# Kernel tuning notes

Hardware: AMD Instinct MI355X
Metric: run time of the kernel (lower is better)

## Reference

```python
import jax, jax.numpy as jnp
import numpy as np

B, N, T, F_IN, H, OUT = 64, 207, 48, 6, 64, 1
RANK = 24  # fixed inner dim of learned adjacency factors


def setup_inputs() -> dict:
    key = jax.random.key(0)
    ks = jax.random.split(key, 10)
    s = lambda k, shp, sc=1.0: jax.random.normal(k, shp, jnp.float32) * sc
    return {
        "x": s(ks[0], (B, N, T, F_IN)),
        "N1": s(ks[1], (N, RANK)),
        "N2": s(ks[2], (RANK, N)),
        "W1": s(ks[3], (F_IN, H), 0.2),
        "b1": jnp.zeros((H,), jnp.float32),
        "W2": s(ks[4], (H, H), 0.1),
        "b2": jnp.zeros((H,), jnp.float32),
        "W_ih": s(ks[5], (4 * H, H), 0.1),
        "W_hh": s(ks[6], (4 * H, H), 0.1),
        "b_ih": jnp.zeros((4 * H,), jnp.float32),
        "b_hh": jnp.zeros((4 * H,), jnp.float32),
        "W_fc": s(ks[7], (H, OUT), 0.1),
        "b_fc": jnp.zeros((OUT,), jnp.float32),
    }


def reference(x, N1, N2, W1, b1, W2, b2, W_ih, W_hh, b_ih, b_hh, W_fc, b_fc):
    Bn, Nn, Tn, Fn = x.shape
    # sigmoid(N1@N2) > 0 everywhere -> dense_to_sparse yields ALL N^2 edges
    # (self-loops included); GCNConv's gcn_norm adds one extra self-loop,
    # edge weights all 1 -> A = ones + I, deg = N+1, symmetric normalization.
    adj = jax.nn.sigmoid(N1 @ N2)
    mask = (adj > 0).astype(x.dtype)  # structurally all-ones
    A = mask + jnp.eye(Nn, dtype=x.dtype)
    dinv = jax.lax.rsqrt(A.sum(axis=1))
    A_hat = dinv[:, None] * A * dinv[None, :]  # [N, N]

    xt = jnp.transpose(x, (0, 2, 1, 3))  # [B, T, N, F]
    # GCNConv: propagate(x @ W) with sym-norm, then bias; relu; dropout=eval no-op
    h = jax.nn.relu(jnp.einsum('mn,btnh->btmh', A_hat, xt @ W1) + b1)
    h = jax.nn.relu(jnp.einsum('mn,btnh->btmh', A_hat, h @ W2) + b2)

    # [B, T, N, H] -> [B*N, T, H] for the LSTM
    seq = jnp.transpose(h, (0, 2, 1, 3)).reshape(Bn * Nn, Tn, -1)
    Hd = W_hh.shape[1]

    def step(carry, x_t):
        h_prev, c_prev = carry
        g = x_t @ W_ih.T + b_ih + h_prev @ W_hh.T + b_hh
        i, f, gg, o = jnp.split(g, 4, axis=-1)  # torch gate order i,f,g,o
        c = jax.nn.sigmoid(f) * c_prev + jax.nn.sigmoid(i) * jnp.tanh(gg)
        h_new = jax.nn.sigmoid(o) * jnp.tanh(c)
        return (h_new, c), None

    h0 = jnp.zeros((Bn * Nn, Hd), x.dtype)
    (hT, _), _ = jax.lax.scan(step, (h0, h0), jnp.transpose(seq, (1, 0, 2)))
    out = hT @ W_fc + b_fc  # [B*N, OUT]
    return out.reshape(Bn, Nn, -1)
```

## Files before the change

kernel.cpp:

```cpp
#include <hip/hip_runtime.h>
#include <math.h>

#define NB 64
#define NN 207
#define NT 48
#define NF 6
#define NH 64
#define NSEQ (NB*NN)
#define NG2  (NSEQ/32)
#define TSU  ((size_t)NSEQ*NH)

typedef short bf8_t __attribute__((ext_vector_type(8)));
typedef float f4_t  __attribute__((ext_vector_type(4)));
typedef unsigned short ushort;
typedef unsigned int uint;

__device__ __forceinline__ ushort bf16h(float x){
  uint u = __float_as_uint(x);
  return (ushort)((u + 0x7FFF + ((u>>16)&1)) >> 16);
}
__device__ __forceinline__ float bf16f(ushort h){
  return __uint_as_float((uint)h << 16);
}
__device__ __forceinline__ float fsig(float x){
  return __builtin_amdgcn_rcpf(1.0f + __expf(-x));
}
__device__ __forceinline__ float ftanh(float x){
  x = fminf(15.0f, fmaxf(-15.0f, x));
  float e = __expf(2.0f*x);
  return 1.0f - 2.0f*__builtin_amdgcn_rcpf(e + 1.0f);
}

__device__ __forceinline__ void lds_barrier(){
  __builtin_amdgcn_sched_barrier(0);
  asm volatile("s_waitcnt lgkmcnt(0)" ::: "memory");
  __builtin_amdgcn_s_barrier();
  __builtin_amdgcn_sched_barrier(0);
}


#define HW 72
#define XS6 40
#define GCN7_LDS_BYTES (208*HW*2 + (207*XS6 + NF*64 + 64 + 64 + 6*64 + 6*64 + 48)*4)

__global__ __launch_bounds__(256, 2) void gcn_kernel(
    const float* __restrict__ x, const float* __restrict__ W1, const float* __restrict__ b1,
    const float* __restrict__ W2, const float* __restrict__ b2,
    ushort* __restrict__ sxh, ushort* __restrict__ sxl)
{
  extern __shared__ char smraw[];
  ushort* h1b = (ushort*)smraw;
  float*  xs6 = (float*)(h1b + 208*HW);
  float*  W1s = xs6 + 207*XS6;
  float*  b1s = W1s + NF*64;
  float*  b2s = b1s + 64;
  float*  S2_ = b2s + 64;
  float*  r1_ = S2_ + 6*64;
  float*  xsA = r1_ + 6*64;

  const int tid = threadIdx.x;
  const int tg = blockIdx.x, b = blockIdx.y;
  const float inv = 1.0f/208.0f;
  const int l = tid & 63;
  const int w = __builtin_amdgcn_readfirstlane(tid >> 6);
  const int col = l & 15, q = l >> 4;
  const int cw = w*16 + col;

  for (int i=tid; i<6*64; i+=256){ S2_[i]=0.f; r1_[i]=0.f; }
  if (tid < 48) xsA[tid] = 0.f;
  if (tid < 72) h1b[207*HW + tid] = 0;

  for (int i=tid;i<NF*64;i+=256) W1s[i]=W1[i];
  if (tid<64){ b1s[tid]=b1[tid]; b2s[tid]=b2[tid]; }
  {
    const float* xb = x + (size_t)b*NN*(NT*NF) + (size_t)tg*36;
    for (int i=tid; i<207*9; i+=256){
      int n = i/9, c = (i - n*9)*4;
      *(float4*)&xs6[n*XS6 + c] = *(const float4*)&xb[(size_t)n*(NT*NF) + c];
    }
  }
  __syncthreads();

  if (tid < 144){
    int tt = tid/24, rem = tid - tt*24, f = rem>>2, p = rem&3;
    float ps = 0.f;
    for (int n=p; n<NN; n+=4) ps += xs6[n*XS6 + tt*6 + f];
    atomicAdd(&xsA[tt*8+f], ps);
  }

  float wtmp[16];
  #pragma unroll
  for (int kc=0;kc<2;kc++)
    #pragma unroll
    for (int j=0;j<8;j++)
      wtmp[kc*8+j] = W2[(size_t)(kc*32 + q*8 + j)*64 + cw];
  bf8_t B2[2];
  #pragma unroll
  for (int kc=0;kc<2;kc++){
    bf8_t ph;
    #pragma unroll
    for (int j=0;j<8;j++) ph[j] = (short)bf16h(wtmp[kc*8+j]);
    B2[kc]=ph;
  }
  __syncthreads();

  const int ht4 = (tid & 15) * 4;
  const int nti = tid >> 4;

  #pragma unroll 1
  for (int tt=0; tt<6; tt++){
    const int t = tg*6 + tt;
    {
      float s1v[4];
      #pragma unroll
      for (int j=0;j<4;j++){
        float a = 0.f;
        #pragma unroll
        for (int f=0;f<NF;f++) a += xsA[tt*8+f]*W1s[f*64 + ht4 + j];
        s1v[j] = a;
      }
      float cs0=0.f, cs1=0.f, cs2=0.f, cs3=0.f;
      #pragma unroll 1
      for (int p=0;p<4;p++){
        int nt = p*16 + nti;
        if (nt < 52){
          #pragma unroll
          for (int i=0;i<4;i++){
            int n = 4*nt+i;
            if (n < NN){
              float a0=0.f,a1=0.f,a2=0.f,a3=0.f;
              #pragma unroll
              for (int f=0;f<NF;f++){
                float xv = xs6[n*XS6 + tt*6 + f];
                float4 wv = *(const float4*)&W1s[f*64 + ht4];
                a0+=xv*wv.x; a1+=xv*wv.y; a2+=xv*wv.z; a3+=xv*wv.w;
              }
              float v0=(a0+s1v[0])*inv + b1s[ht4+0]; v0 = v0>0.f?v0:0.f;
              float v1=(a1+s1v[1])*inv + b1s[ht4+1]; v1 = v1>0.f?v1:0.f;
              float v2=(a2+s1v[2])*inv + b1s[ht4+2]; v2 = v2>0.f?v2:0.f;
              float v3=(a3+s1v[3])*inv + b1s[ht4+3]; v3 = v3>0.f?v3:0.f;
              ushort4 hi;
              hi.x=bf16h(v0); hi.y=bf16h(v1); hi.z=bf16h(v2); hi.w=bf16h(v3);
              *(ushort4*)&h1b[n*HW + ht4] = hi;
              cs0+=v0; cs1+=v1; cs2+=v2; cs3+=v3;
            }
          }
        }
      }
      atomicAdd(&r1_[tt*64+ht4+0], cs0);
      atomicAdd(&r1_[tt*64+ht4+1], cs1);
      atomicAdd(&r1_[tt*64+ht4+2], cs2);
      atomicAdd(&r1_[tt*64+ht4+3], cs3);
    }
    __syncthreads();

    {
      int h = tid & 63, pp = tid >> 6;
      float ps = 0.f;
      #pragma unroll
      for (int k=0;k<16;k++) ps += r1_[tt*64+pp*16+k]*W2[(size_t)(pp*16+k)*64 + h];
      atomicAdd(&S2_[tt*64+h], ps);
    }

    f4_t acc[13];
    #pragma unroll
    for (int mt=0;mt<13;mt++){ f4_t z; z[0]=0.f;z[1]=0.f;z[2]=0.f;z[3]=0.f; acc[mt]=z; }
    #pragma unroll 2
    for (int mt=0;mt<13;mt++){
      #pragma unroll
      for (int kc=0;kc<2;kc++){
        bf8_t ah = *(const bf8_t*)(h1b + (mt*16+col)*HW + kc*32 + q*8);
        acc[mt] = __builtin_amdgcn_mfma_f32_16x16x32_bf16(ah, B2[kc], acc[mt], 0,0,0);
      }
    }
    __syncthreads();

    {
      const float s2v = S2_[tt*64+cw], b2v = b2s[cw];
      const size_t obase = (size_t)t*TSU + (size_t)(b*NN)*NH + cw;
      #pragma unroll
      for (int mt=0;mt<13;mt++){
        #pragma unroll
        for (int r=0;r<4;r++){
          int n = mt*16 + q*4 + r;
          if (n < NN){
            float v = (acc[mt][r] + s2v)*inv + b2v;
            v = v>0.f ? v : 0.f;
            ushort hb = bf16h(v);
            sxh[obase + (size_t)n*NH] = hb;
            sxl[obase + (size_t)n*NH] = bf16h(v - bf16f(hb));
          }
        }
      }
    }
  }
}

#define HS2 72

__global__ __launch_bounds__(256, 2) void lstm19_kernel(
    const ushort* __restrict__ sxh, const ushort* __restrict__ sxl,
    const float* __restrict__ Wih, const float* __restrict__ Whh,
    const float* __restrict__ bih, const float* __restrict__ bhh,
    const float* __restrict__ Wfc, const float* __restrict__ bfc, float* __restrict__ out)
{
  __shared__ __align__(16) ushort hhp[2][2][16*HS2 + 8];
  __shared__ __align__(16) ushort hlp[2][2][16*HS2 + 8];
  __shared__ __align__(16) ushort xst[2][2][2][2][512];

  const int tid = threadIdx.x;
  const int l = tid & 63;
  const int w = __builtin_amdgcn_readfirstlane(tid >> 6);
  const int col = l & 15, q = l >> 4;
  const int g = blockIdx.x;

  bf8_t Bh[4][4], Bl[4][4];
  #pragma unroll
  for (int mat=0; mat<2; mat++){
    const float* W = mat ? Whh : Wih;
    #pragma unroll
    for (int ty=0; ty<4; ty++){
      #pragma unroll
      for (int kk=0; kk<2; kk++){
        const float* wp = W + (size_t)(ty*64 + w*16 + col)*64 + kk*32 + q*8;
        bf8_t ph, pl2;
        #pragma unroll
        for (int j=0;j<8;j++){
          float wv = wp[j];
          ushort hb = bf16h(wv);
          ph[j] = (short)hb;
          pl2[j] = (short)bf16h(wv - bf16f(hb));
        }
        Bh[ty][mat*2+kk] = ph;
        Bl[ty][mat*2+kk] = pl2;
      }
    }
  }
  float bias[4];
  #pragma unroll
  for (int ty=0;ty<4;ty++){
    int r = ty*64 + w*16 + col;
    bias[ty] = bih[r] + bhh[r];
  }
  float c[2][4];
  #pragma unroll
  for (int s=0;s<2;s++)
    #pragma unroll
    for (int i=0;i<4;i++) c[s][i]=0.f;

  for (int i=tid; i<16*HS2; i+=256){
    hhp[0][0][i]=0; hhp[0][1][i]=0; hlp[0][0][i]=0; hlp[0][1][i]=0;
  }

  const int ss = w >> 1, pl = w & 1;
  const ushort* xsrc = (pl ? sxl : sxh) + (size_t)(g*32 + ss*16 + col)*64 + (size_t)(q*8);

  #pragma unroll
  for (int t2=0; t2<2; t2++){
    bf8_t a0 = *(const bf8_t*)(xsrc + (size_t)t2*TSU);
    bf8_t a1 = *(const bf8_t*)(xsrc + (size_t)t2*TSU + 32);
    *(bf8_t*)&xst[t2][ss][pl][0][l*8] = a0;
    *(bf8_t*)&xst[t2][ss][pl][1][l*8] = a1;
  }

  const int d = w*16 + col;
  __syncthreads();

  #pragma unroll 2
  for (int t=0; t<NT; t++){
    const int cur = t & 1;

    bf8_t g0, g1;
    const bool do_stage = (t+2 < NT);
    if (do_stage){
      g0 = *(const bf8_t*)(xsrc + (size_t)(t+2)*TSU);
      g1 = *(const bf8_t*)(xsrc + (size_t)(t+2)*TSU + 32);
    }

    bf8_t xh0[2], xh1[2], xl0[2], xl1[2];
    #pragma unroll
    for (int s=0;s<2;s++){
      xh0[s] = *(const bf8_t*)&xst[cur][s][0][0][l*8];
      xh1[s] = *(const bf8_t*)&xst[cur][s][0][1][l*8];
      xl0[s] = *(const bf8_t*)&xst[cur][s][1][0][l*8];
      xl1[s] = *(const bf8_t*)&xst[cur][s][1][1][l*8];
    }

    f4_t acc[2][4];
    #pragma unroll
    for (int s=0;s<2;s++)
      #pragma unroll
      for (int ty=0;ty<4;ty++){ f4_t z; z[0]=bias[ty];z[1]=bias[ty];z[2]=bias[ty];z[3]=bias[ty]; acc[s][ty]=z; }
    #pragma unroll
    for (int s=0;s<2;s++)
      #pragma unroll
      for (int ty=0;ty<4;ty++){
        acc[s][ty] = __builtin_amdgcn_mfma_f32_16x16x32_bf16(xh0[s], Bh[ty][0], acc[s][ty], 0,0,0);
        acc[s][ty] = __builtin_amdgcn_mfma_f32_16x16x32_bf16(xl0[s], Bh[ty][0], acc[s][ty], 0,0,0);
        acc[s][ty] = __builtin_amdgcn_mfma_f32_16x16x32_bf16(xh0[s], Bl[ty][0], acc[s][ty], 0,0,0);
        acc[s][ty] = __builtin_amdgcn_mfma_f32_16x16x32_bf16(xh1[s], Bh[ty][1], acc[s][ty], 0,0,0);
        acc[s][ty] = __builtin_amdgcn_mfma_f32_16x16x32_bf16(xl1[s], Bh[ty][1], acc[s][ty], 0,0,0);
        acc[s][ty] = __builtin_amdgcn_mfma_f32_16x16x32_bf16(xh1[s], Bl[ty][1], acc[s][ty], 0,0,0);
      }

    lds_barrier();

    bf8_t hh0[2], hh1[2], hl0[2], hl1[2];
    #pragma unroll
    for (int s=0;s<2;s++){
      const ushort* ph = &hhp[cur][s][0] + col*HS2 + q*8;
      const ushort* pl2 = &hlp[cur][s][0] + col*HS2 + q*8;
      hh0[s] = *(const bf8_t*)(ph);
      hh1[s] = *(const bf8_t*)(ph + 32);
      hl0[s] = *(const bf8_t*)(pl2);
      hl1[s] = *(const bf8_t*)(pl2 + 32);
    }
    #pragma unroll
    for (int s=0;s<2;s++)
      #pragma unroll
      for (int ty=0;ty<4;ty++){
        acc[s][ty] = __builtin_amdgcn_mfma_f32_16x16x32_bf16(hh0[s], Bh[ty][2], acc[s][ty], 0,0,0);
        acc[s][ty] = __builtin_amdgcn_mfma_f32_16x16x32_bf16(hl0[s], Bh[ty][2], acc[s][ty], 0,0,0);
        acc[s][ty] = __builtin_amdgcn_mfma_f32_16x16x32_bf16(hh0[s], Bl[ty][2], acc[s][ty], 0,0,0);
        acc[s][ty] = __builtin_amdgcn_mfma_f32_16x16x32_bf16(hh1[s], Bh[ty][3], acc[s][ty], 0,0,0);
        acc[s][ty] = __builtin_amdgcn_mfma_f32_16x16x32_bf16(hl1[s], Bh[ty][3], acc[s][ty], 0,0,0);
        acc[s][ty] = __builtin_amdgcn_mfma_f32_16x16x32_bf16(hh1[s], Bl[ty][3], acc[s][ty], 0,0,0);
      }

    if (do_stage){
      *(bf8_t*)&xst[cur][ss][pl][0][l*8] = g0;
      *(bf8_t*)&xst[cur][ss][pl][1][l*8] = g1;
    }

    #pragma unroll
    for (int s=0;s<2;s++){
      ushort* wh = &hhp[cur^1][s][0];
      ushort* wl = &hlp[cur^1][s][0];
      float hv[4];
      #pragma unroll
      for (int r=0;r<4;r++){
        float ig = fsig(acc[s][0][r]);
        float fg = fsig(acc[s][1][r]);
        float gt = ftanh(acc[s][2][r]);
        float og = fsig(acc[s][3][r]);
        float cc = fg*c[s][r] + ig*gt;
        c[s][r] = cc;
        hv[r] = og*ftanh(cc);
      }
      const int o0 = (q*4)*HS2 + d;
      if (t != NT-1){
        uint ph01, ph23, pl01, pl23;
        asm("v_cvt_pk_bf16_f32 %0, %1, %2" : "=v"(ph01) : "v"(hv[0]), "v"(hv[1]));
        asm("v_cvt_pk_bf16_f32 %0, %1, %2" : "=v"(ph23) : "v"(hv[2]), "v"(hv[3]));
        float r0 = hv[0] - __uint_as_float(ph01 << 16);
        float r1 = hv[1] - __uint_as_float(ph01 & 0xffff0000u);
        float r2 = hv[2] - __uint_as_float(ph23 << 16);
        float r3 = hv[3] - __uint_as_float(ph23 & 0xffff0000u);
        asm("v_cvt_pk_bf16_f32 %0, %1, %2" : "=v"(pl01) : "v"(r0), "v"(r1));
        asm("v_cvt_pk_bf16_f32 %0, %1, %2" : "=v"(pl23) : "v"(r2), "v"(r3));
        wh[o0]         = (ushort)ph01;
        wh[o0 + HS2]   = (ushort)(ph01 >> 16);
        wh[o0 + 2*HS2] = (ushort)ph23;
        wh[o0 + 3*HS2] = (ushort)(ph23 >> 16);
        wl[o0]         = (ushort)pl01;
        wl[o0 + HS2]   = (ushort)(pl01 >> 16);
        wl[o0 + 2*HS2] = (ushort)pl23;
        wl[o0 + 3*HS2] = (ushort)(pl23 >> 16);
      } else {
        #pragma unroll
        for (int r=0;r<4;r++){
          uint bits = __float_as_uint(hv[r]);
          wh[o0 + r*HS2] = (ushort)(bits >> 16);
          wl[o0 + r*HS2] = (ushort)(bits & 0xffffu);
        }
      }
    }
  }
  __syncthreads();

  if (tid < 32){
    const int s = tid >> 4, r = tid & 15;
    float a = bfc[0];
    const ushort* fh = &hhp[NT&1][s][0] + r*HS2;
    const ushort* fl = &hlp[NT&1][s][0] + r*HS2;
    #pragma unroll 8
    for (int k=0;k<64;k++){
      float v = __uint_as_float(((uint)fh[k] << 16) | (uint)fl[k]);
      a += v * Wfc[k];
    }
    out[g*32 + tid] = a;
  }
}

extern "C" void kernel_launch(void* const* d_in, const int* in_sizes, int n_in,
                              void* d_out, int out_size, void* d_ws, size_t ws_size,
                              hipStream_t stream) {
  const float* x   = (const float*)d_in[0];
  const float* W1  = (const float*)d_in[3];
  const float* b1  = (const float*)d_in[4];
  const float* W2  = (const float*)d_in[5];
  const float* b2  = (const float*)d_in[6];
  const float* Wih = (const float*)d_in[7];
  const float* Whh = (const float*)d_in[8];
  const float* bih = (const float*)d_in[9];
  const float* bhh = (const float*)d_in[10];
  const float* Wfc = (const float*)d_in[11];
  const float* bfc = (const float*)d_in[12];

  ushort* sxh = (ushort*)d_ws;
  ushort* sxl = sxh + (size_t)NT*TSU;
  float*  out = (float*)d_out;

  hipFuncSetAttribute((const void*)gcn_kernel, hipFuncAttributeMaxDynamicSharedMemorySize, GCN7_LDS_BYTES);

  gcn_kernel<<<dim3(NT/6, NB), 256, GCN7_LDS_BYTES, stream>>>(x, W1, b1, W2, b2, sxh, sxl);
  lstm19_kernel<<<NG2, 256, 0, stream>>>(sxh, sxl, Wih, Whh, bih, bhh, Wfc, bfc, out);
}
```

Baseline: 304.5 us.

## Process 64 sequences per LSTM block instead of 32

The LSTM kernel now gives each 256-thread block four 16-sequence subtiles (64 sequences) instead of two, and launches half as many blocks (207 instead of 414). Each wave stages both the high and low bf16 planes of its own subtile and runs twice as many MFMAs per timestep with the same register-resident weight fragments. This amortizes the per-step barrier and the weight preload over more work and gives more independent MFMA chains to hide latency. The cost is more registers (launch bounds drop to 1 block/SM) and fewer blocks, which may leave CUs idle on a 256-CU part.

```diff
diff --git a/kernel.cpp b/kernel.cpp
--- a/kernel.cpp
+++ b/kernel.cpp
@@ -7,7 +7,7 @@
 #define NF 6
 #define NH 64
 #define NSEQ (NB*NN)
-#define NG2  (NSEQ/32)
+#define NG4  (NSEQ/64)
 #define TSU  ((size_t)NSEQ*NH)
 
 typedef short bf8_t __attribute__((ext_vector_type(8)));
@@ -198,15 +198,15 @@
 
 #define HS2 72
 
-__global__ __launch_bounds__(256, 2) void lstm19_kernel(
+__global__ __launch_bounds__(256, 1) void lstm20_kernel(
     const ushort* __restrict__ sxh, const ushort* __restrict__ sxl,
     const float* __restrict__ Wih, const float* __restrict__ Whh,
     const float* __restrict__ bih, const float* __restrict__ bhh,
     const float* __restrict__ Wfc, const float* __restrict__ bfc, float* __restrict__ out)
 {
-  __shared__ __align__(16) ushort hhp[2][2][16*HS2 + 8];
-  __shared__ __align__(16) ushort hlp[2][2][16*HS2 + 8];
-  __shared__ __align__(16) ushort xst[2][2][2][2][512];
+  __shared__ __align__(16) ushort hhp[2][4][16*HS2 + 8];
+  __shared__ __align__(16) ushort hlp[2][4][16*HS2 + 8];
+  __shared__ __align__(16) ushort xst[2][4][2][2][512];
 
   const int tid = threadIdx.x;
   const int l = tid & 63;
@@ -242,25 +242,30 @@
     int r = ty*64 + w*16 + col;
     bias[ty] = bih[r] + bhh[r];
   }
-  float c[2][4];
-  #pragma unroll
-  for (int s=0;s<2;s++)
+  float c[4][4];
+  #pragma unroll
+  for (int s=0;s<4;s++)
     #pragma unroll
     for (int i=0;i<4;i++) c[s][i]=0.f;
 
   for (int i=tid; i<16*HS2; i+=256){
-    hhp[0][0][i]=0; hhp[0][1][i]=0; hlp[0][0][i]=0; hlp[0][1][i]=0;
-  }
-
-  const int ss = w >> 1, pl = w & 1;
-  const ushort* xsrc = (pl ? sxl : sxh) + (size_t)(g*32 + ss*16 + col)*64 + (size_t)(q*8);
+    #pragma unroll
+    for (int s=0;s<4;s++){ hhp[0][s][i]=0; hlp[0][s][i]=0; }
+  }
+
+  const ushort* xsh = sxh + (size_t)(g*64 + w*16 + col)*64 + (size_t)(q*8);
+  const ushort* xsl = sxl + (size_t)(g*64 + w*16 + col)*64 + (size_t)(q*8);
 
   #pragma unroll
   for (int t2=0; t2<2; t2++){
-    bf8_t a0 = *(const bf8_t*)(xsrc + (size_t)t2*TSU);
-    bf8_t a1 = *(const bf8_t*)(xsrc + (size_t)t2*TSU + 32);
-    *(bf8_t*)&xst[t2][ss][pl][0][l*8] = a0;
-    *(bf8_t*)&xst[t2][ss][pl][1][l*8] = a1;
+    bf8_t h0 = *(const bf8_t*)(xsh + (size_t)t2*TSU);
+    bf8_t h1 = *(const bf8_t*)(xsh + (size_t)t2*TSU + 32);
+    bf8_t l0 = *(const bf8_t*)(xsl + (size_t)t2*TSU);
+    bf8_t l1 = *(const bf8_t*)(xsl + (size_t)t2*TSU + 32);
+    *(bf8_t*)&xst[t2][w][0][0][l*8] = h0;
+    *(bf8_t*)&xst[t2][w][0][1][l*8] = h1;
+    *(bf8_t*)&xst[t2][w][1][0][l*8] = l0;
+    *(bf8_t*)&xst[t2][w][1][1][l*8] = l1;
   }
 
   const int d = w*16 + col;
@@ -270,70 +275,67 @@
   for (int t=0; t<NT; t++){
     const int cur = t & 1;
 
-    bf8_t g0, g1;
+    bf8_t gh0, gh1, gl0, gl1;
     const bool do_stage = (t+2 < NT);
     if (do_stage){
-      g0 = *(const bf8_t*)(xsrc + (size_t)(t+2)*TSU);
-      g1 = *(const bf8_t*)(xsrc + (size_t)(t+2)*TSU + 32);
-    }
-
-    bf8_t xh0[2], xh1[2], xl0[2], xl1[2];
-    #pragma unroll
-    for (int s=0;s<2;s++){
-      xh0[s] = *(const bf8_t*)&xst[cur][s][0][0][l*8];
-      xh1[s] = *(const bf8_t*)&xst[cur][s][0][1][l*8];
-      xl0[s] = *(const bf8_t*)&xst[cur][s][1][0][l*8];
-      xl1[s] = *(const bf8_t*)&xst[cur][s][1][1][l*8];
-    }
-
-    f4_t acc[2][4];
-    #pragma unroll
-    for (int s=0;s<2;s++)
+      gh0 = *(const bf8_t*)(xsh + (size_t)(t+2)*TSU);
+      gh1 = *(const bf8_t*)(xsh + (size_t)(t+2)*TSU + 32);
+      gl0 = *(const bf8_t*)(xsl + (size_t)(t+2)*TSU);
+      gl1 = *(const bf8_t*)(xsl + (size_t)(t+2)*TSU + 32);
+    }
+
+    f4_t acc[4][4];
+    #pragma unroll
+    for (int s=0;s<4;s++)
       #pragma unroll
       for (int ty=0;ty<4;ty++){ f4_t z; z[0]=bias[ty];z[1]=bias[ty];z[2]=bias[ty];z[3]=bias[ty]; acc[s][ty]=z; }
     #pragma unroll
-    for (int s=0;s<2;s++)
+    for (int s=0;s<4;s++){
+      bf8_t xh0 = *(const bf8_t*)&xst[cur][s][0][0][l*8];
+      bf8_t xh1 = *(const bf8_t*)&xst[cur][s][0][1][l*8];
+      bf8_t xl0 = *(const bf8_t*)&xst[cur][s][1][0][l*8];
+      bf8_t xl1 = *(const bf8_t*)&xst[cur][s][1][1][l*8];
       #pragma unroll
       for (int ty=0;ty<4;ty++){
-        acc[s][ty] = __builtin_amdgcn_mfma_f32_16x16x32_bf16(xh0[s], Bh[ty][0], acc[s][ty], 0,0,0);
-        acc[s][ty] = __builtin_amdgcn_mfma_f32_16x16x32_bf16(xl0[s], Bh[ty][0], acc[s][ty], 0,0,0);
-        acc[s][ty] = __builtin_amdgcn_mfma_f32_16x16x32_bf16(xh0[s], Bl[ty][0], acc[s][ty], 0,0,0);
-        acc[s][ty] = __builtin_amdgcn_mfma_f32_16x16x32_bf16(xh1[s], Bh[ty][1], acc[s][ty], 0,0,0);
-        acc[s][ty] = __builtin_amdgcn_mfma_f32_16x16x32_bf16(xl1[s], Bh[ty][1], acc[s][ty], 0,0,0);
-        acc[s][ty] = __builtin_amdgcn_mfma_f32_16x16x32_bf16(xh1[s], Bl[ty][1], acc[s][ty], 0,0,0);
-      }
+        acc[s][ty] = __builtin_amdgcn_mfma_f32_16x16x32_bf16(xh0, Bh[ty][0], acc[s][ty], 0,0,0);
+        acc[s][ty] = __builtin_amdgcn_mfma_f32_16x16x32_bf16(xl0, Bh[ty][0], acc[s][ty], 0,0,0);
+        acc[s][ty] = __builtin_amdgcn_mfma_f32_16x16x32_bf16(xh0, Bl[ty][0], acc[s][ty], 0,0,0);
+        acc[s][ty] = __builtin_amdgcn_mfma_f32_16x16x32_bf16(xh1, Bh[ty][1], acc[s][ty], 0,0,0);
+        acc[s][ty] = __builtin_amdgcn_mfma_f32_16x16x32_bf16(xl1, Bh[ty][1], acc[s][ty], 0,0,0);
+        acc[s][ty] = __builtin_amdgcn_mfma_f32_16x16x32_bf16(xh1, Bl[ty][1], acc[s][ty], 0,0,0);
+      }
+    }
 
     lds_barrier();
 
-    bf8_t hh0[2], hh1[2], hl0[2], hl1[2];
-    #pragma unroll
-    for (int s=0;s<2;s++){
+    #pragma unroll
+    for (int s=0;s<4;s++){
       const ushort* ph = &hhp[cur][s][0] + col*HS2 + q*8;
       const ushort* pl2 = &hlp[cur][s][0] + col*HS2 + q*8;
-      hh0[s] = *(const bf8_t*)(ph);
-      hh1[s] = *(const bf8_t*)(ph + 32);
-      hl0[s] = *(const bf8_t*)(pl2);
-      hl1[s] = *(const bf8_t*)(pl2 + 32);
-    }
-    #pragma unroll
-    for (int s=0;s<2;s++)
+      bf8_t hh0 = *(const bf8_t*)(ph);
+      bf8_t hh1 = *(const bf8_t*)(ph + 32);
+      bf8_t hl0 = *(const bf8_t*)(pl2);
+      bf8_t hl1 = *(const bf8_t*)(pl2 + 32);
       #pragma unroll
       for (int ty=0;ty<4;ty++){
-        acc[s][ty] = __builtin_amdgcn_mfma_f32_16x16x32_bf16(hh0[s], Bh[ty][2], acc[s][ty], 0,0,0);
-        acc[s][ty] = __builtin_amdgcn_mfma_f32_16x16x32_bf16(hl0[s], Bh[ty][2], acc[s][ty], 0,0,0);
-        acc[s][ty] = __builtin_amdgcn_mfma_f32_16x16x32_bf16(hh0[s], Bl[ty][2], acc[s][ty], 0,0,0);
-        acc[s][ty] = __builtin_amdgcn_mfma_f32_16x16x32_bf16(hh1[s], Bh[ty][3], acc[s][ty], 0,0,0);
-        acc[s][ty] = __builtin_amdgcn_mfma_f32_16x16x32_bf16(hl1[s], Bh[ty][3], acc[s][ty], 0,0,0);
-        acc[s][ty] = __builtin_amdgcn_mfma_f32_16x16x32_bf16(hh1[s], Bl[ty][3], acc[s][ty], 0,0,0);
-      }
+        acc[s][ty] = __builtin_amdgcn_mfma_f32_16x16x32_bf16(hh0, Bh[ty][2], acc[s][ty], 0,0,0);
+        acc[s][ty] = __builtin_amdgcn_mfma_f32_16x16x32_bf16(hl0, Bh[ty][2], acc[s][ty], 0,0,0);
+        acc[s][ty] = __builtin_amdgcn_mfma_f32_16x16x32_bf16(hh0, Bl[ty][2], acc[s][ty], 0,0,0);
+        acc[s][ty] = __builtin_amdgcn_mfma_f32_16x16x32_bf16(hh1, Bh[ty][3], acc[s][ty], 0,0,0);
+        acc[s][ty] = __builtin_amdgcn_mfma_f32_16x16x32_bf16(hl1, Bh[ty][3], acc[s][ty], 0,0,0);
+        acc[s][ty] = __builtin_amdgcn_mfma_f32_16x16x32_bf16(hh1, Bl[ty][3], acc[s][ty], 0,0,0);
+      }
+    }
 
     if (do_stage){
-      *(bf8_t*)&xst[cur][ss][pl][0][l*8] = g0;
-      *(bf8_t*)&xst[cur][ss][pl][1][l*8] = g1;
-    }
-
-    #pragma unroll
-    for (int s=0;s<2;s++){
+      *(bf8_t*)&xst[cur][w][0][0][l*8] = gh0;
+      *(bf8_t*)&xst[cur][w][0][1][l*8] = gh1;
+      *(bf8_t*)&xst[cur][w][1][0][l*8] = gl0;
+      *(bf8_t*)&xst[cur][w][1][1][l*8] = gl1;
+    }
+
+    #pragma unroll
+    for (int s=0;s<4;s++){
       ushort* wh = &hhp[cur^1][s][0];
       ushort* wl = &hlp[cur^1][s][0];
       float hv[4];
@@ -378,7 +380,7 @@
   }
   __syncthreads();
 
-  if (tid < 32){
+  if (tid < 64){
     const int s = tid >> 4, r = tid & 15;
     float a = bfc[0];
     const ushort* fh = &hhp[NT&1][s][0] + r*HS2;
@@ -388,7 +390,7 @@
       float v = __uint_as_float(((uint)fh[k] << 16) | (uint)fl[k]);
       a += v * Wfc[k];
     }
-    out[g*32 + tid] = a;
+    out[g*64 + tid] = a;
   }
 }
 
@@ -414,5 +416,5 @@
   hipFuncSetAttribute((const void*)gcn_kernel, hipFuncAttributeMaxDynamicSharedMemorySize, GCN7_LDS_BYTES);
 
   gcn_kernel<<<dim3(NT/6, NB), 256, GCN7_LDS_BYTES, stream>>>(x, W1, b1, W2, b2, sxh, sxl);
-  lstm19_kernel<<<NG2, 256, 0, stream>>>(sxh, sxl, Wih, Whh, bih, bhh, Wfc, bfc, out);
-}
+  lstm20_kernel<<<NG4, 256, 0, stream>>>(sxh, sxl, Wih, Whh, bih, bhh, Wfc, bfc, out);
+}
```

After: 313.2 us. 1.03x slower.
